# Performance work log

Measured on AMD Instinct MI355X. Metric: run time of the kernel, lower is better.

## Reference

```python
import jax, jax.numpy as jnp
import numpy as np
from jax import lax

B, N, W, L, H = 8, 1024, 1024, 12, 16
EPS = 1e-5


def setup_inputs() -> dict:
    key = jax.random.key(0)
    ks = jax.random.split(key, 14)
    std = 0.25 / np.sqrt(W)  # init_scale * sqrt(1/width)
    inp = {
        "x": jax.random.normal(ks[0], (B, N, W), dtype=jnp.float32),
        # stacked per-layer params, leading dim L
        "ln1_g": jnp.ones((L, W), jnp.float32),
        "ln1_b": jnp.zeros((L, W), jnp.float32),
        "w_qkv": jax.random.normal(ks[1], (L, W, 3 * W), jnp.float32) * std,
        "b_qkv": jnp.zeros((L, 3 * W), jnp.float32),
        "w_o":   jax.random.normal(ks[2], (L, W, W), jnp.float32) * std,
        "b_o":   jnp.zeros((L, W), jnp.float32),
        "ln2_g": jnp.ones((L, W), jnp.float32),
        "ln2_b": jnp.zeros((L, W), jnp.float32),
        "w_fc":  jax.random.normal(ks[3], (L, W, 4 * W), jnp.float32) * std,
        "b_fc":  jnp.zeros((L, 4 * W), jnp.float32),
        "w_pr":  jax.random.normal(ks[4], (L, 4 * W, W), jnp.float32) * std,
        "b_pr":  jnp.zeros((L, W), jnp.float32),
    }
    return inp


def _layernorm(x, g, b):
    mu = jnp.mean(x, axis=-1, keepdims=True)
    var = jnp.mean(jnp.square(x - mu), axis=-1, keepdims=True)
    return (x - mu) * lax.rsqrt(var + EPS) * g + b


def _attention(qkv, heads):
    # qkv: [B, N, 3W]; matches QKVMultiheadAttention exactly
    bs, n_ctx, width3 = qkv.shape
    attn_ch = width3 // heads // 3
    scale = 1.0 / np.sqrt(np.sqrt(attn_ch))
    qkv = qkv.reshape(bs, n_ctx, heads, 3 * attn_ch)
    q, k, v = jnp.split(qkv, 3, axis=-1)  # each [B,N,H,c]
    w = jnp.einsum("bthc,bshc->bhts", q * scale, k * scale)
    w = jax.nn.softmax(w.astype(jnp.float32), axis=-1).astype(qkv.dtype)
    out = jnp.einsum("bhts,bshc->bthc", w, v)
    return out.reshape(bs, n_ctx, heads * attn_ch)


def reference(x, ln1_g, ln1_b, w_qkv, b_qkv, w_o, b_o,
              ln2_g, ln2_b, w_fc, b_fc, w_pr, b_pr):
    params = (ln1_g, ln1_b, w_qkv, b_qkv, w_o, b_o,
              ln2_g, ln2_b, w_fc, b_fc, w_pr, b_pr)

    def step(h, p):
        (g1, bb1, wqkv, bqkv, wo, bo, g2, bb2, wfc, bfc, wpr, bpr) = p
        a = _layernorm(h, g1, bb1)
        a = jnp.einsum("bnw,wk->bnk", a, wqkv) + bqkv
        a = _attention(a, H)
        a = jnp.einsum("bnw,wk->bnk", a, wo) + bo
        h = h + a
        m = _layernorm(h, g2, bb2)
        m = jax.nn.gelu(jnp.einsum("bnw,wf->bnf", m, wfc) + bfc, approximate=False)
        m = jnp.einsum("bnf,fw->bnw", m, wpr) + bpr
        return h + m, None

    out, _ = lax.scan(step, x, params)
    return out
```

## Files before the change

### kernel.cpp

```cpp
#include <hip/hip_runtime.h>
#include <cstdint>
#include <cstddef>

#define WDIM 1024
#define BDIM 8
#define NDIM 1024
#define LDIM 12
#define HDIM 16
#define MROWS (BDIM * NDIM)

using bf16x8 = __attribute__((ext_vector_type(8))) __bf16;
using f32x4  = __attribute__((ext_vector_type(4))) float;
using u16x8  = __attribute__((ext_vector_type(8))) ushort;

static __device__ __forceinline__ f32x4 mfma16(bf16x8 a, bf16x8 b, f32x4 c) {
  return __builtin_amdgcn_mfma_f32_16x16x32_bf16(a, b, c, 0, 0, 0);
}

static __device__ __forceinline__ ushort f2bf(float f) {
  uint32_t u = __builtin_bit_cast(uint32_t, f);
  u = (u + 0x7FFFu + ((u >> 16) & 1u)) >> 16;
  return (ushort)u;
}

static __device__ __forceinline__ void g2lds16(const void* g, void* l) {
  __builtin_amdgcn_global_load_lds(
      (__attribute__((address_space(1))) void*)(g),
      (__attribute__((address_space(3))) void*)(l), 16, 0, 0);
}

__global__ __launch_bounds__(256) void ln_kernel(const float* __restrict__ h,
                                                 const float* __restrict__ g,
                                                 const float* __restrict__ b,
                                                 ushort* __restrict__ out) {
  const int w = threadIdx.x >> 6, l = threadIdx.x & 63;
  const int row = blockIdx.x * 4 + w;
  const float4* rp = (const float4*)(h + (size_t)row * WDIM);
  float4 v[4];
  float s = 0.f, s2 = 0.f;
  #pragma unroll
  for (int j = 0; j < 4; ++j) {
    v[j] = rp[j * 64 + l];
    s  += v[j].x + v[j].y + v[j].z + v[j].w;
    s2 += v[j].x * v[j].x + v[j].y * v[j].y + v[j].z * v[j].z + v[j].w * v[j].w;
  }
  #pragma unroll
  for (int off = 32; off; off >>= 1) {
    s  += __shfl_xor(s, off);
    s2 += __shfl_xor(s2, off);
  }
  const float mu   = s * (1.0f / WDIM);
  const float var  = s2 * (1.0f / WDIM) - mu * mu;
  const float rstd = rsqrtf(var + 1e-5f);
  ushort4* op = (ushort4*)(out + (size_t)row * WDIM);
  #pragma unroll
  for (int j = 0; j < 4; ++j) {
    const float4 gv = ((const float4*)g)[j * 64 + l];
    const float4 bv = ((const float4*)b)[j * 64 + l];
    ushort4 o;
    o.x = f2bf((v[j].x - mu) * rstd * gv.x + bv.x);
    o.y = f2bf((v[j].y - mu) * rstd * gv.y + bv.y);
    o.z = f2bf((v[j].z - mu) * rstd * gv.z + bv.z);
    o.w = f2bf((v[j].w - mu) * rstd * gv.w + bv.w);
    op[j * 64 + l] = o;
  }
}

__global__ __launch_bounds__(256) void transpose_cvt(const float* __restrict__ in,
                                                     ushort* __restrict__ out,
                                                     int K, int N) {
  __shared__ float sm[32][33];
  const int n0 = blockIdx.x * 32, k0 = blockIdx.y * 32;
  const int tx = threadIdx.x, ty = threadIdx.y;
  #pragma unroll
  for (int j = 0; j < 4; ++j)
    sm[ty + j * 8][tx] = in[(size_t)(k0 + ty + j * 8) * N + n0 + tx];
  __syncthreads();
  #pragma unroll
  for (int j = 0; j < 4; ++j)
    out[(size_t)(n0 + ty + j * 8) * K + k0 + tx] = f2bf(sm[tx][ty + j * 8]);
}

__global__ __launch_bounds__(256) void v_transpose(const ushort* __restrict__ qkv,
                                                   ushort* __restrict__ vT) {
  const int nb = blockIdx.x, bh = blockIdx.y;
  const int b = bh >> 4, h = bh & 15;
  const int tid = threadIdx.x;
  __shared__ ushort smT[64 * 64];
  const int n0 = nb * 64;
  const size_t rowb = (size_t)b * NDIM;
  #pragma unroll
  for (int p = 0; p < 2; ++p) {
    const int n  = p * 32 + (tid >> 3);
    const int d0 = (tid & 7) * 8;
    const uint4 vv = *(const uint4*)(qkv + (rowb + n0 + n) * 3072 + h * 192 + 128 + d0);
    const ushort* e = (const ushort*)&vv;
    const int key = d0;
    #pragma unroll
    for (int j = 0; j < 8; ++j)
      smT[(d0 + j) * 64 + (n ^ key)] = e[j];
  }
  __syncthreads();
  #pragma unroll
  for (int p = 0; p < 2; ++p) {
    const int d  = p * 32 + (tid >> 3);
    const int nc = (tid & 7) * 8;
    const int key = (d >> 3) << 3;
    const uint4 ov = *(const uint4*)&smT[d * 64 + (nc ^ key)];
    *(uint4*)(vT + ((size_t)bh * 64 + d) * NDIM + n0 + nc) = ov;
  }
}

enum { EPI_BF16 = 0, EPI_RES = 1, EPI_GELU = 2 };

template <int EPI>
__global__ __launch_bounds__(512, 2) void gemm256_kernel(
    const ushort* __restrict__ A, const ushort* __restrict__ Bt,
    const float* __restrict__ bias, ushort* __restrict__ outb,
    int M, int N, int K) {
  __shared__ ushort smA[2 * 2 * 256 * 32];
  __shared__ ushort smB[2 * 2 * 256 * 32];
  const int tid = threadIdx.x;
  const int w = tid >> 6, l = tid & 63;
  const int lr = l & 15, lg = l >> 4;
  const int wm = w >> 2, wn = w & 3;

  const int gx = gridDim.x;
  const int nwg = gx * gridDim.y;
  const int id0 = blockIdx.y * gx + blockIdx.x;
  const int id = (id0 & 7) * (nwg >> 3) + (id0 >> 3);
  const int row0 = (id / gx) * 256, col0 = (id % gx) * 256;

  const int KT = K >> 6;
  const int srow_l = l >> 2;
  const int scol = (((l & 3) ^ ((l >> 3) & 3)) * 8);
  const int ks = ((lg ^ ((lr >> 1) & 3)) * 8);

  f32x4 acc[8][4] = {};

  auto stageA = [&](int tau, int hh) {
    const int base = (((tau & 1) * 2 + hh) * 8192);
    const int colb = tau * 64 + hh * 32 + scol;
    #pragma unroll
    for (int j = 0; j < 2; ++j) {
      const int c = j * 8 + w;
      g2lds16(A + (size_t)(row0 + 16 * c + srow_l) * K + colb, &smA[base + c * 512]);
    }
  };
  auto stageB = [&](int tau, int hh) {
    const int base = (((tau & 1) * 2 + hh) * 8192);
    const int colb = tau * 64 + hh * 32 + scol;
    #pragma unroll
    for (int j = 0; j < 2; ++j) {
      const int c = j * 8 + w;
      g2lds16(Bt + (size_t)(col0 + 16 * c + srow_l) * K + colb, &smB[base + c * 512]);
    }
  };

  stageA(0, 0); stageB(0, 0);
  stageA(0, 1); stageB(0, 1);
  stageA(1, 0); stageB(1, 0);
  asm volatile("s_waitcnt vmcnt(8)" ::: "memory");
  __builtin_amdgcn_sched_barrier(0);
  __builtin_amdgcn_s_barrier();

  for (int tau = 0; tau < KT; ++tau) {
    const int ab0 = (tau & 1) * 16384;
    const int ab1 = ab0 + 8192;
    bf16x8 af[8], bf0, bf1;

    #pragma unroll
    for (int m = 0; m < 8; ++m)
      af[m] = *(const bf16x8*)&smA[ab0 + (wm * 128 + m * 16 + lr) * 32 + ks];
    bf0 = *(const bf16x8*)&smB[ab0 + (wn * 64 + lr) * 32 + ks];
    bf1 = *(const bf16x8*)&smB[ab0 + (wn * 64 + 16 + lr) * 32 + ks];
    if (tau + 1 < KT) stageA(tau + 1, 1);
    __builtin_amdgcn_s_barrier();
    asm volatile("s_waitcnt lgkmcnt(0)" ::: "memory");
    __builtin_amdgcn_sched_barrier(0);
    __builtin_amdgcn_s_setprio(1);
    #pragma unroll
    for (int m = 0; m < 8; ++m) {
      acc[m][0] = mfma16(af[m], bf0, acc[m][0]);
      acc[m][1] = mfma16(af[m], bf1, acc[m][1]);
    }
    __builtin_amdgcn_s_setprio(0);
    __builtin_amdgcn_s_barrier();

    bf0 = *(const bf16x8*)&smB[ab0 + (wn * 64 + 32 + lr) * 32 + ks];
    bf1 = *(const bf16x8*)&smB[ab0 + (wn * 64 + 48 + lr) * 32 + ks];
    if (tau + 1 < KT) stageB(tau + 1, 1);
    __builtin_amdgcn_s_barrier();
    asm volatile("s_waitcnt lgkmcnt(0)" ::: "memory");
    __builtin_amdgcn_sched_barrier(0);
    __builtin_amdgcn_s_setprio(1);
    #pragma unroll
    for (int m = 0; m < 8; ++m) {
      acc[m][2] = mfma16(af[m], bf0, acc[m][2]);
      acc[m][3] = mfma16(af[m], bf1, acc[m][3]);
    }
    __builtin_amdgcn_s_setprio(0);
    if (tau + 1 < KT) { asm volatile("s_waitcnt vmcnt(8)" ::: "memory"); }
    else              { asm volatile("s_waitcnt vmcnt(0)" ::: "memory"); }
    __builtin_amdgcn_sched_barrier(0);
    __builtin_amdgcn_s_barrier();

    #pragma unroll
    for (int m = 0; m < 8; ++m)
      af[m] = *(const bf16x8*)&smA[ab1 + (wm * 128 + m * 16 + lr) * 32 + ks];
    bf0 = *(const bf16x8*)&smB[ab1 + (wn * 64 + lr) * 32 + ks];
    bf1 = *(const bf16x8*)&smB[ab1 + (wn * 64 + 16 + lr) * 32 + ks];
    if (tau + 2 < KT) { stageA(tau + 2, 0); stageB(tau + 2, 0); }
    __builtin_amdgcn_s_barrier();
    asm volatile("s_waitcnt lgkmcnt(0)" ::: "memory");
    __builtin_amdgcn_sched_barrier(0);
    __builtin_amdgcn_s_setprio(1);
    #pragma unroll
    for (int m = 0; m < 8; ++m) {
      acc[m][0] = mfma16(af[m], bf0, acc[m][0]);
      acc[m][1] = mfma16(af[m], bf1, acc[m][1]);
    }
    __builtin_amdgcn_s_setprio(0);
    __builtin_amdgcn_s_barrier();

    bf0 = *(const bf16x8*)&smB[ab1 + (wn * 64 + 32 + lr) * 32 + ks];
    bf1 = *(const bf16x8*)&smB[ab1 + (wn * 64 + 48 + lr) * 32 + ks];
    __builtin_amdgcn_s_barrier();
    asm volatile("s_waitcnt lgkmcnt(0)" ::: "memory");
    __builtin_amdgcn_sched_barrier(0);
    __builtin_amdgcn_s_setprio(1);
    #pragma unroll
    for (int m = 0; m < 8; ++m) {
      acc[m][2] = mfma16(af[m], bf0, acc[m][2]);
      acc[m][3] = mfma16(af[m], bf1, acc[m][3]);
    }
    __builtin_amdgcn_s_setprio(0);
    if (tau + 2 < KT)      { asm volatile("s_waitcnt vmcnt(8)" ::: "memory"); }
    else if (tau + 1 < KT) { asm volatile("s_waitcnt vmcnt(4)" ::: "memory"); }
    __builtin_amdgcn_sched_barrier(0);
    __builtin_amdgcn_s_barrier();
  }

  #pragma unroll
  for (int m = 0; m < 8; ++m) {
    #pragma unroll
    for (int n = 0; n < 4; ++n) {
      #pragma unroll
      for (int i = 0; i < 4; ++i) {
        const int r = row0 + wm * 128 + m * 16 + lg * 4 + i;
        const int c = col0 + wn * 64 + n * 16 + lr;
        float v = acc[m][n][i] + bias[c];
        if constexpr (EPI == EPI_GELU) {
          v = 0.5f * v * (1.0f + erff(v * 0.70710678118f));
        }
        outb[(size_t)r * N + c] = f2bf(v);
      }
    }
  }
}

template <int EPI>
__global__ __launch_bounds__(256) void gemm_kernel(
    const ushort* __restrict__ A, const ushort* __restrict__ Bt,
    const float* __restrict__ bias, float* __restrict__ resid,
    ushort* __restrict__ outb, int M, int N, int K) {
  __shared__ ushort smA[2][128 * 64];
  __shared__ ushort smB[2][128 * 64];
  const int tid = threadIdx.x;
  const int w = tid >> 6, l = tid & 63;
  const int lr = l & 15, lg = l >> 4;
  const int wr = (w >> 1) * 64, wc = (w & 1) * 64;

  const int gx = gridDim.x;
  const int nwg = gx * gridDim.y;
  const int id0 = blockIdx.y * gx + blockIdx.x;
  const int id = (id0 & 7) * (nwg >> 3) + (id0 >> 3);
  const int row0 = (id / gx) * 128, col0 = (id % gx) * 128;

  const int srow = tid >> 3;
  const int sslot = tid & 7;
  f32x4 acc[4][4] = {};
  const int KT = K >> 6;

  auto stage = [&](int buf, int kt) {
    const int kb = kt << 6;
    #pragma unroll
    for (int j = 0; j < 4; ++j) {
      const int r = j * 32 + srow;
      const int sc = ((sslot ^ (r & 7)) * 8);
      g2lds16(A  + (size_t)(row0 + r) * K + kb + sc, &smA[buf][j * 2048 + w * 512]);
      g2lds16(Bt + (size_t)(col0 + r) * K + kb + sc, &smB[buf][j * 2048 + w * 512]);
    }
  };

  stage(0, 0);
  int cur = 0;
  for (int kt = 0; kt < KT; ++kt) {
    __syncthreads();
    if (kt + 1 < KT) stage(cur ^ 1, kt + 1);
    bf16x8 af[2][4], bfr[2][4];
    const int rs = lr & 7;
    #pragma unroll
    for (int kk = 0; kk < 2; ++kk) {
      #pragma unroll
      for (int t = 0; t < 4; ++t) {
        const int k8 = (kk * 4 + lg) ^ rs;
        af[kk][t]  = *(const bf16x8*)&smA[cur][(wr + t * 16 + lr) * 64 + k8 * 8];
        bfr[kk][t] = *(const bf16x8*)&smB[cur][(wc + t * 16 + lr) * 64 + k8 * 8];
      }
    }
    __builtin_amdgcn_s_setprio(1);
    #pragma unroll
    for (int kk = 0; kk < 2; ++kk)
      #pragma unroll
      for (int mt = 0; mt < 4; ++mt)
        #pragma unroll
        for (int nt = 0; nt < 4; ++nt)
          acc[mt][nt] = mfma16(af[kk][mt], bfr[kk][nt], acc[mt][nt]);
    __builtin_amdgcn_s_setprio(0);
    cur ^= 1;
  }

  #pragma unroll
  for (int mt = 0; mt < 4; ++mt) {
    #pragma unroll
    for (int nt = 0; nt < 4; ++nt) {
      #pragma unroll
      for (int i = 0; i < 4; ++i) {
        const int r = row0 + wr + mt * 16 + lg * 4 + i;
        const int c = col0 + wc + nt * 16 + lr;
        float v = acc[mt][nt][i] + bias[c];
        if constexpr (EPI == EPI_RES) {
          resid[(size_t)r * N + c] += v;
        } else if constexpr (EPI == EPI_GELU) {
          const float gg = 0.5f * v * (1.0f + erff(v * 0.70710678118f));
          outb[(size_t)r * N + c] = f2bf(gg);
        } else {
          outb[(size_t)r * N + c] = f2bf(v);
        }
      }
    }
  }
}

__global__ __launch_bounds__(512) void attn_kernel(const ushort* __restrict__ qkv,
                                                   const ushort* __restrict__ vT,
                                                   ushort* __restrict__ out) {
  const int qb = blockIdx.x;
  const int bh = blockIdx.y;
  const int b = bh >> 4, h = bh & 15;
  const int tid = threadIdx.x;
  const int w = tid >> 6, l = tid & 63;
  const int lr = l & 15, lg = l >> 4;
  __shared__ ushort smK[2][64 * 64];
  __shared__ ushort smV[2][64 * 64];
  __shared__ ushort smP[8][16 * 64];
  const int q0 = qb * 128 + w * 16;
  const size_t rowb = (size_t)b * NDIM;
  const ushort* vhead = vT + (size_t)bh * 64 * NDIM;
  ushort* P = smP[w];

  const u16x8 ob = {0x3F80, 0x3F80, 0x3F80, 0x3F80, 0x3F80, 0x3F80, 0x3F80, 0x3F80};
  const bf16x8 onesv = __builtin_bit_cast(bf16x8, ob);

  const int srow = l >> 3;
  const int scol = ((l & 7) ^ srow) * 8;
  const ushort* kg = qkv + (rowb + w * 8 + srow) * 3072 + h * 192 + 64 + scol;
  const ushort* vg = vhead + (size_t)(w * 8 + srow) * NDIM + scol;

  auto stage = [&](int buf, int kb) {
    g2lds16(kg + (size_t)kb * 64 * 3072, &smK[buf][w * 512]);
    g2lds16(vg + kb * 64,                &smV[buf][w * 512]);
  };

  bf16x8 qf0, qf1;
  {
    const ushort* qp = qkv + (rowb + q0 + lr) * 3072 + h * 192;
    qf0 = *(const bf16x8*)(qp + lg * 8);
    qf1 = *(const bf16x8*)(qp + 32 + lg * 8);
  }
  f32x4 o[4] = {};
  f32x4 lacc = {0.f, 0.f, 0.f, 0.f};

  stage(0, 0);
  int cur = 0;
  for (int kb = 0; kb < NDIM / 64; ++kb) {
    __syncthreads();
    if (kb + 1 < NDIM / 64) stage(cur ^ 1, kb + 1);

    const int rs = lr & 7;
    f32x4 s[4];
    #pragma unroll
    for (int kt = 0; kt < 4; ++kt) {
      const ushort* krow = &smK[cur][(kt * 16 + lr) * 64];
      const bf16x8 kf0 = *(const bf16x8*)&krow[(lg ^ rs) * 8];
      const bf16x8 kf1 = *(const bf16x8*)&krow[((4 + lg) ^ rs) * 8];
      f32x4 z = {0.f, 0.f, 0.f, 0.f};
      s[kt] = mfma16(qf1, kf1, mfma16(qf0, kf0, z));
    }

    #pragma unroll
    for (int i = 0; i < 4; ++i) {
      const int row = lg * 4 + i;
      const int swz = (row & 7) << 3;
      ushort* pr = P + row * 64;
      pr[lr ^ swz]        = f2bf(__expf(s[0][i] * 0.125f));
      pr[(16 + lr) ^ swz] = f2bf(__expf(s[1][i] * 0.125f));
      pr[(32 + lr) ^ swz] = f2bf(__expf(s[2][i] * 0.125f));
      pr[(48 + lr) ^ swz] = f2bf(__expf(s[3][i] * 0.125f));
    }

    const int rswz = rs << 3;
    const bf16x8 pf0 = *(const bf16x8*)&P[lr * 64 + ((lg * 8) ^ rswz)];
    const bf16x8 pf1 = *(const bf16x8*)&P[lr * 64 + ((32 + lg * 8) ^ rswz)];
    lacc = mfma16(pf0, onesv, mfma16(pf1, onesv, lacc));
    #pragma unroll
    for (int dt = 0; dt < 4; ++dt) {
      const ushort* vrow = &smV[cur][(dt * 16 + lr) * 64];
      const bf16x8 vf0 = *(const bf16x8*)&vrow[(lg ^ rs) * 8];
      const bf16x8 vf1 = *(const bf16x8*)&vrow[((4 + lg) ^ rs) * 8];
      o[dt] = mfma16(pf0, vf0, mfma16(pf1, vf1, o[dt]));
    }
    cur ^= 1;
  }

  #pragma unroll
  for (int i = 0; i < 4; ++i) {
    const float inv = 1.0f / lacc[i];
    const size_t orow = (rowb + q0 + lg * 4 + i) * (size_t)WDIM;
    #pragma unroll
    for (int dt = 0; dt < 4; ++dt)
      out[orow + h * 64 + dt * 16 + lr] = f2bf(o[dt][i] * inv);
  }
}

extern "C" void kernel_launch(void* const* d_in, const int* in_sizes, int n_in,
                              void* d_out, int out_size, void* d_ws, size_t ws_size,
                              hipStream_t stream) {
  const float* x     = (const float*)d_in[0];
  const float* ln1_g = (const float*)d_in[1];
  const float* ln1_b = (const float*)d_in[2];
  const float* w_qkv = (const float*)d_in[3];
  const float* b_qkv = (const float*)d_in[4];
  const float* w_o   = (const float*)d_in[5];
  const float* b_o   = (const float*)d_in[6];
  const float* ln2_g = (const float*)d_in[7];
  const float* ln2_b = (const float*)d_in[8];
  const float* w_fc  = (const float*)d_in[9];
  const float* b_fc  = (const float*)d_in[10];
  const float* w_pr  = (const float*)d_in[11];
  const float* b_pr  = (const float*)d_in[12];

  float* hbuf = (float*)d_out;

  uint8_t* p = (uint8_t*)d_ws;
  ushort* wqkv_t = (ushort*)p; p += (size_t)3072 * 1024 * 2;
  ushort* wo_t   = (ushort*)p; p += (size_t)1024 * 1024 * 2;
  ushort* wfc_t  = (ushort*)p; p += (size_t)4096 * 1024 * 2;
  ushort* wpr_t  = (ushort*)p; p += (size_t)1024 * 4096 * 2;
  ushort* lnb    = (ushort*)p; p += (size_t)MROWS * 1024 * 2;
  ushort* qkvb   = (ushort*)p; p += (size_t)MROWS * 3072 * 2;
  ushort* attnb  = (ushort*)p; p += (size_t)MROWS * 1024 * 2;
  ushort* mlpb   = (ushort*)p; p += (size_t)MROWS * 4096 * 2;
  ushort* vTb    = (ushort*)p; p += (size_t)BDIM * HDIM * 64 * NDIM * 2;

  hipMemcpyAsync(hbuf, x, (size_t)MROWS * WDIM * sizeof(float),
                 hipMemcpyDeviceToDevice, stream);

  for (int l = 0; l < LDIM; ++l) {
    ln_kernel<<<MROWS / 4, 256, 0, stream>>>(hbuf, ln1_g + l * 1024, ln1_b + l * 1024, lnb);
    transpose_cvt<<<dim3(96, 32), dim3(32, 8), 0, stream>>>(
        w_qkv + (size_t)l * 1024 * 3072, wqkv_t, 1024, 3072);
    gemm256_kernel<EPI_BF16><<<dim3(12, 32), 512, 0, stream>>>(
        lnb, wqkv_t, b_qkv + (size_t)l * 3072, qkvb, MROWS, 3072, 1024);
    v_transpose<<<dim3(16, 128), 256, 0, stream>>>(qkvb, vTb);
    attn_kernel<<<dim3(8, 128), 512, 0, stream>>>(qkvb, vTb, attnb);
    transpose_cvt<<<dim3(32, 32), dim3(32, 8), 0, stream>>>(
        w_o + (size_t)l * 1024 * 1024, wo_t, 1024, 1024);
    gemm_kernel<EPI_RES><<<dim3(8, 64), 256, 0, stream>>>(
        attnb, wo_t, b_o + (size_t)l * 1024, hbuf, nullptr, MROWS, 1024, 1024);
    ln_kernel<<<MROWS / 4, 256, 0, stream>>>(hbuf, ln2_g + l * 1024, ln2_b + l * 1024, lnb);
    transpose_cvt<<<dim3(128, 32), dim3(32, 8), 0, stream>>>(
        w_fc + (size_t)l * 1024 * 4096, wfc_t, 1024, 4096);
    gemm256_kernel<EPI_GELU><<<dim3(16, 32), 512, 0, stream>>>(
        lnb, wfc_t, b_fc + (size_t)l * 4096, mlpb, MROWS, 4096, 1024);
    transpose_cvt<<<dim3(32, 128), dim3(32, 8), 0, stream>>>(
        w_pr + (size_t)l * 4096 * 1024, wpr_t, 4096, 1024);
    gemm_kernel<EPI_RES><<<dim3(8, 64), 256, 0, stream>>>(
        mlpb, wpr_t, b_pr + (size_t)l * 1024, hbuf, nullptr, MROWS, 1024, 4096);
  }
}
```

Measured before the change: 4.509 ms.

## Keep attention probabilities in registers by transposing QK^T and permuting key rows

Computes the score tile as K·Q^T with a permuted key-row mapping so each lane's accumulator outputs line up with the A-operand layout of the PV MFMA. Probabilities are packed with v_cvt_pk_bf16_f32 directly into bf16x8 registers, which removes the per-wave LDS round trip through smP. The LDS swizzle for K/V staging is changed to match the new row mapping. The aim is to cut LDS writes and reads and the conversion cost in the attention inner loop, at the cost of more intricate index arithmetic that must stay consistent between the K and V swizzles.

New measurement: 4.442 ms. Within noise of the previous version (-1.5%).

```diff
diff --git a/kernel.cpp b/kernel.cpp
--- a/kernel.cpp
+++ b/kernel.cpp
@@ -11,6 +11,7 @@
 
 using bf16x8 = __attribute__((ext_vector_type(8))) __bf16;
 using f32x4  = __attribute__((ext_vector_type(4))) float;
+using u32x4  = __attribute__((ext_vector_type(4))) uint32_t;
 using u16x8  = __attribute__((ext_vector_type(8))) ushort;
 
 static __device__ __forceinline__ f32x4 mfma16(bf16x8 a, bf16x8 b, f32x4 c) {
@@ -21,6 +22,12 @@
   uint32_t u = __builtin_bit_cast(uint32_t, f);
   u = (u + 0x7FFFu + ((u >> 16) & 1u)) >> 16;
   return (ushort)u;
+}
+
+static __device__ __forceinline__ uint32_t cvtpk(float lo, float hi) {
+  uint32_t r;
+  asm("v_cvt_pk_bf16_f32 %0, %1, %2" : "=v"(r) : "v"(lo), "v"(hi));
+  return r;
 }
 
 static __device__ __forceinline__ void g2lds16(const void* g, void* l) {
@@ -354,17 +361,16 @@
   const int lr = l & 15, lg = l >> 4;
   __shared__ ushort smK[2][64 * 64];
   __shared__ ushort smV[2][64 * 64];
-  __shared__ ushort smP[8][16 * 64];
   const int q0 = qb * 128 + w * 16;
   const size_t rowb = (size_t)b * NDIM;
   const ushort* vhead = vT + (size_t)bh * 64 * NDIM;
-  ushort* P = smP[w];
 
   const u16x8 ob = {0x3F80, 0x3F80, 0x3F80, 0x3F80, 0x3F80, 0x3F80, 0x3F80, 0x3F80};
   const bf16x8 onesv = __builtin_bit_cast(bf16x8, ob);
 
   const int srow = l >> 3;
-  const int scol = ((l & 7) ^ srow) * 8;
+  const int skey = (srow & 3) ^ ((w & 1) << 2);
+  const int scol = ((l & 7) ^ skey) * 8;
   const ushort* kg = qkv + (rowb + w * 8 + srow) * 3072 + h * 192 + 64 + scol;
   const ushort* vg = vhead + (size_t)(w * 8 + srow) * NDIM + scol;
 
@@ -382,44 +388,50 @@
   f32x4 o[4] = {};
   f32x4 lacc = {0.f, 0.f, 0.f, 0.f};
 
+  const int rbase = (lr >> 2) * 8 + (lr & 3);
+  const int kkey  = (lr & 3) ^ (((lr >> 2) & 1) << 2);
+  const int vkey  = (lr & 3) ^ (((lr >> 3) & 1) << 2);
+  const int kp0 = (lg ^ kkey) * 8, kp1 = ((4 + lg) ^ kkey) * 8;
+  const int vp0 = (lg ^ vkey) * 8, vp1 = ((4 + lg) ^ vkey) * 8;
+
   stage(0, 0);
   int cur = 0;
   for (int kb = 0; kb < NDIM / 64; ++kb) {
     __syncthreads();
     if (kb + 1 < NDIM / 64) stage(cur ^ 1, kb + 1);
 
-    const int rs = lr & 7;
-    f32x4 s[4];
-    #pragma unroll
-    for (int kt = 0; kt < 4; ++kt) {
-      const ushort* krow = &smK[cur][(kt * 16 + lr) * 64];
-      const bf16x8 kf0 = *(const bf16x8*)&krow[(lg ^ rs) * 8];
-      const bf16x8 kf1 = *(const bf16x8*)&krow[((4 + lg) ^ rs) * 8];
-      f32x4 z = {0.f, 0.f, 0.f, 0.f};
-      s[kt] = mfma16(qf1, kf1, mfma16(qf0, kf0, z));
-    }
-
-    #pragma unroll
-    for (int i = 0; i < 4; ++i) {
-      const int row = lg * 4 + i;
-      const int swz = (row & 7) << 3;
-      ushort* pr = P + row * 64;
-      pr[lr ^ swz]        = f2bf(__expf(s[0][i] * 0.125f));
-      pr[(16 + lr) ^ swz] = f2bf(__expf(s[1][i] * 0.125f));
-      pr[(32 + lr) ^ swz] = f2bf(__expf(s[2][i] * 0.125f));
-      pr[(48 + lr) ^ swz] = f2bf(__expf(s[3][i] * 0.125f));
-    }
-
-    const int rswz = rs << 3;
-    const bf16x8 pf0 = *(const bf16x8*)&P[lr * 64 + ((lg * 8) ^ rswz)];
-    const bf16x8 pf1 = *(const bf16x8*)&P[lr * 64 + ((32 + lg * 8) ^ rswz)];
-    lacc = mfma16(pf0, onesv, mfma16(pf1, onesv, lacc));
+    f32x4 s[2][2];
+    #pragma unroll
+    for (int hh = 0; hh < 2; ++hh) {
+      #pragma unroll
+      for (int m = 0; m < 2; ++m) {
+        const int r = hh * 32 + rbase + 4 * m;
+        const ushort* kr = &smK[cur][r * 64];
+        const bf16x8 kf0 = *(const bf16x8*)&kr[kp0];
+        const bf16x8 kf1 = *(const bf16x8*)&kr[kp1];
+        f32x4 z = {0.f, 0.f, 0.f, 0.f};
+        s[hh][m] = mfma16(kf1, qf1, mfma16(kf0, qf0, z));
+      }
+    }
+
+    bf16x8 pf[2];
+    #pragma unroll
+    for (int hh = 0; hh < 2; ++hh) {
+      u32x4 pk;
+      pk[0] = cvtpk(__expf(s[hh][0][0] * 0.125f), __expf(s[hh][0][1] * 0.125f));
+      pk[1] = cvtpk(__expf(s[hh][0][2] * 0.125f), __expf(s[hh][0][3] * 0.125f));
+      pk[2] = cvtpk(__expf(s[hh][1][0] * 0.125f), __expf(s[hh][1][1] * 0.125f));
+      pk[3] = cvtpk(__expf(s[hh][1][2] * 0.125f), __expf(s[hh][1][3] * 0.125f));
+      pf[hh] = __builtin_bit_cast(bf16x8, pk);
+    }
+
+    lacc = mfma16(pf[0], onesv, mfma16(pf[1], onesv, lacc));
     #pragma unroll
     for (int dt = 0; dt < 4; ++dt) {
       const ushort* vrow = &smV[cur][(dt * 16 + lr) * 64];
-      const bf16x8 vf0 = *(const bf16x8*)&vrow[(lg ^ rs) * 8];
-      const bf16x8 vf1 = *(const bf16x8*)&vrow[((4 + lg) ^ rs) * 8];
-      o[dt] = mfma16(pf0, vf0, mfma16(pf1, vf1, o[dt]));
+      const bf16x8 vf0 = *(const bf16x8*)&vrow[vp0];
+      const bf16x8 vf1 = *(const bf16x8*)&vrow[vp1];
+      o[dt] = mfma16(pf[0], vf0, mfma16(pf[1], vf1, o[dt]));
     }
     cur ^= 1;
   }
```
